# Kernel tuning notes

Measured on AMD Instinct MI355X. Metric: run time of the kernel, lower is better.

The kernel has to match this reference:

```python
import jax, jax.numpy as jnp
import numpy as np

B, N_PER, DEG = 1024, 256, 16
N = B * N_PER            # 262144 total nodes
E = B * N_PER * DEG      # 4194304 edges
F_IN, H, K, C = 7, 64, 50, 2


def setup_inputs() -> dict:
    key = jax.random.key(0)
    ks = jax.random.split(key, 16)
    rng = np.random.default_rng(0)
    # within-graph random edges: nodes of graph g occupy [g*N_PER, (g+1)*N_PER)
    offs = np.repeat(np.arange(B, dtype=np.int64) * N_PER, N_PER * DEG)
    src = offs + rng.integers(0, N_PER, size=E)
    dst = offs + rng.integers(0, N_PER, size=E)
    edge_index = jnp.asarray(np.stack([src, dst]), dtype=jnp.int64)
    batch = jnp.repeat(jnp.arange(B, dtype=jnp.int64), N_PER)
    sc = lambda fan: 1.0 / np.sqrt(fan)
    return {
        'x': jax.random.normal(ks[0], (N, F_IN), jnp.float32),
        'W1a': jax.random.normal(ks[1], (F_IN, H), jnp.float32) * sc(F_IN),
        'b1a': jnp.zeros((H,), jnp.float32),
        'W1b': jax.random.normal(ks[2], (H, H), jnp.float32) * sc(H),
        'b1b': jnp.zeros((H,), jnp.float32),
        'Wp': jax.random.normal(ks[3], (H, K), jnp.float32) * sc(H),
        'bp': jnp.zeros((K,), jnp.float32),
        'W2a': jax.random.normal(ks[4], (H, H), jnp.float32) * sc(H),
        'b2a': jnp.zeros((H,), jnp.float32),
        'W2b': jax.random.normal(ks[5], (H, H), jnp.float32) * sc(H),
        'b2b': jnp.zeros((H,), jnp.float32),
        'Wl': jax.random.normal(ks[6], (H, C), jnp.float32) * sc(H),
        'bl': jnp.zeros((C,), jnp.float32),
        'edge_index': edge_index,
        'batch': batch,
    }


def reference(x, W1a, b1a, W1b, b1b, Wp, bp, W2a, b2a, W2b, b2b, Wl, bl,
              edge_index, batch):
    src, dst = edge_index[0], edge_index[1]
    # --- sparse GINConv (eps=0): MLP(x + sum_{j in N(i)} x_j) ---
    agg = jnp.zeros_like(x).at[dst].add(x[src])          # scatter-add over edges
    h = jax.nn.relu((x + agg) @ W1a + b1a) @ W1b + b1b   # [N, H]
    # --- densify per graph (equal-size contiguous graphs) ---
    xd = h.reshape(B, N_PER, H)                          # [B, n, H]
    g = src // N_PER
    si = src % N_PER
    di = dst % N_PER
    A = jnp.zeros((B, N_PER, N_PER), x.dtype).at[g, si, di].add(1.0)
    # --- BNPool-style soft cluster pooling ---
    S = jax.nn.softmax(xd @ Wp + bp, axis=-1)            # [B, n, K]
    xp = jnp.einsum('bnk,bnd->bkd', S, xd)               # [B, K, H]
    AS = jnp.einsum('bnm,bmk->bnk', A, S)
    Ap = jnp.einsum('bnk,bnl->bkl', S, AS)               # [B, K, K]
    SSt = jnp.einsum('bnk,bmk->bnm', S, S)
    link_loss = jnp.sqrt(jnp.sum((A - SSt) ** 2)) / A.size
    ent_loss = -jnp.mean(jnp.sum(S * jnp.log(S + 1e-15), axis=-1))
    aux_loss = link_loss + ent_loss
    # --- DenseGINConv (eps=0): MLP(x + A @ x) ---
    h2 = xp + jnp.einsum('bkl,bld->bkd', Ap, xp)
    h2 = jax.nn.relu(h2 @ W2a + b2a) @ W2b + b2b         # [B, K, H]
    # --- mean pool over clusters + classifier ---
    logits = h2.mean(axis=1) @ Wl + bl                   # [B, C]
    return jax.nn.log_softmax(logits, axis=-1), aux_loss
```

## Files before the change

### kernel.cpp

```cpp
#include <hip/hip_runtime.h>
#include <math.h>

#define NG   1024
#define NP   256
#define EPG  4096
#define ETOT 4194304
#define FIN  7
#define HD   64
#define KC   50
#define FST  72
#define TST  264
#define AST2 132
#define TSC  0.00390625f
#define TSCI 256.0f

#define SW_ST(k, n)  ((k) * 256 + ((n) ^ (((k) & 7) << 3)))
#define SW_AW(r, w)  ((r) * 128 + ((w) ^ (((r) & 7) << 2)))
#define SW_AH(r, h)  ((r) * 256 + ((h) ^ (((r) & 7) << 3)))


typedef __attribute__((ext_vector_type(8))) _Float16 v8h;
typedef __attribute__((ext_vector_type(4))) float v4f;

__global__ void finalize_k(const float* __restrict__ ws, float* __restrict__ out) {
    if (threadIdx.x == 0) {
        float num = ws[0] - 2.f * ws[2] + ws[3];
        float link = sqrtf(fmaxf(num, 0.f)) / 67108864.0f;
        float ent  = -ws[1] / 262144.0f;
        out[2048] = link + ent;
    }
}

__device__ __forceinline__ float blockReduceN(float v, float* red, int nw) {
    __syncthreads();
    #pragma unroll
    for (int o = 32; o > 0; o >>= 1) v += __shfl_down(v, o);
    if ((threadIdx.x & 63) == 0) red[threadIdx.x >> 6] = v;
    __syncthreads();
    float r = 0.f;
    if (threadIdx.x == 0) {
        for (int i = 0; i < nw; ++i) r += red[i];
    }
    return r;
}

__device__ __forceinline__ void blockReduce3(float& a, float& b, float& c,
                                             float* red) {
    __syncthreads();
    #pragma unroll
    for (int o = 32; o > 0; o >>= 1) {
        a += __shfl_down(a, o);
        b += __shfl_down(b, o);
        c += __shfl_down(c, o);
    }
    const int wid = threadIdx.x >> 6;
    if ((threadIdx.x & 63) == 0) {
        red[wid * 3] = a; red[wid * 3 + 1] = b; red[wid * 3 + 2] = c;
    }
    __syncthreads();
    if (threadIdx.x == 0) {
        float ra = 0.f, rb = 0.f, rc = 0.f;
        for (int i = 0; i < 16; ++i) {
            ra += red[i * 3]; rb += red[i * 3 + 1]; rc += red[i * 3 + 2];
        }
        a = ra; b = rb; c = rc;
    }
}

__launch_bounds__(1024, 1)
__global__ void mega(const int* __restrict__ esrc, const int* __restrict__ edst,
                     const float* __restrict__ x,
                     const float* __restrict__ W1a, const float* __restrict__ b1a,
                     const float* __restrict__ W1b, const float* __restrict__ b1b,
                     const float* __restrict__ Wp,  const float* __restrict__ bp,
                     const float* __restrict__ W2a, const float* __restrict__ b2a,
                     const float* __restrict__ W2b, const float* __restrict__ b2b,
                     const float* __restrict__ Wl,  const float* __restrict__ bl,
                     float* __restrict__ out, float* __restrict__ ws)
{
    __shared__ __align__(16) _Float16 ST[64 * 256];
    __shared__ __align__(16) _Float16 xagg[NP * 8];
    __shared__ __align__(16) _Float16 W1bT[64 * FST];
    __shared__ __align__(16) _Float16 WWT[64 * FST];
    __shared__ __align__(16) _Float16 W2aT[64 * FST];
    __shared__ __align__(16) _Float16 W2bT[64 * FST];
    __shared__ float bPl[64];
    __shared__ __align__(16) union {
        struct {
            unsigned char ssi[EPG];
            float xt8[NP * 8];
            unsigned int hist[256], cur[256], roff[NP + 1];
        } k1;
        struct {
            unsigned char pad[16384];
            _Float16 WpT_s[64 * FST];
            _Float16 W1bN[64 * FST];
        } w;
        struct {
            _Float16 t1b[NP * FST];
            _Float16 t1T[HD * TST];
        } k2;
        struct {
            unsigned int cnt[128 * 128];
            _Float16 T1T[64 * AST2];
        } a;
        struct {
            _Float16 Apf_tf[64 * FST];
            _Float16 xpT[64 * FST];
            _Float16 h2f[64 * FST];
        } b;
    } u;
    __shared__ float cs[64];
    __shared__ float red[48];

    const int g = blockIdx.x, tid = threadIdx.x;
    const int lane = tid & 63, wid = tid >> 6;
    const int l15 = lane & 15, quad = lane >> 4, fko = quad * 8;
    const int mt = (wid >> 2) << 4, nt = (wid & 3) << 4;

    for (int i = tid; i < 64 * 128; i += 1024) ((unsigned int*)ST)[i] = 0u;
    for (int i = tid; i < 64 * FST / 2; i += 1024) ((unsigned int*)u.w.WpT_s)[i] = 0u;
    if (tid < 256) u.k1.hist[tid] = 0u;
    __syncthreads();

    unsigned int cellr[4];
    #pragma unroll
    for (int j = 0; j < 4; ++j) {
        int e = tid + j * 1024;
        int s = esrc[g * EPG + e] & (NP - 1);
        int d = edst[g * EPG + e] & (NP - 1);
        cellr[j] = (unsigned)((s << 8) | d);
        atomicAdd(&u.k1.hist[d], 1u);
    }
    for (int i = tid; i < NP * 8; i += 1024) {
        int n = i >> 3, f = i & 7;
        u.k1.xt8[i] = (f < FIN) ? x[g * NP * FIN + n * FIN + f] : 0.f;
    }
    #pragma unroll
    for (int j = 0; j < 4; ++j) {
        int i = tid + j * 1024;
        int a0 = i >> 6, b0 = i & 63;
        W1bT[b0 * FST + a0] = (_Float16)W1b[i];
        u.w.W1bN[a0 * FST + b0] = (_Float16)W1b[i];
        W2aT[b0 * FST + a0] = (_Float16)W2a[i];
        W2bT[b0 * FST + a0] = (_Float16)W2b[i];
    }
    for (int i = tid; i < HD * KC; i += 1024) {
        int h2 = i / KC, k = i - h2 * KC;
        u.w.WpT_s[k * FST + h2] = (_Float16)Wp[i];
    }
    __syncthreads();

    if (wid == 0) {
        unsigned carry = 0;
        for (int c = 0; c < 4; ++c) {
            unsigned v = u.k1.hist[c * 64 + lane];
            unsigned s = v;
            #pragma unroll
            for (int o = 1; o < 64; o <<= 1) {
                unsigned t = __shfl_up(s, o);
                if (lane >= o) s += t;
            }
            unsigned excl = s - v + carry;
            u.k1.roff[c * 64 + lane] = excl;
            u.k1.cur[c * 64 + lane] = excl;
            carry += __shfl(s, 63);
        }
        if (lane == 0) u.k1.roff[NP] = EPG;
    }
    {
        v4f acc = {0.f, 0.f, 0.f, 0.f};
        #pragma unroll
        for (int ks = 0; ks < 2; ++ks) {
            v8h af = *(const v8h*)&u.w.WpT_s[(mt + l15) * FST + ks * 32 + fko];
            v8h bf = *(const v8h*)&u.w.W1bN[(nt + l15) * FST + ks * 32 + fko];
            acc = __builtin_amdgcn_mfma_f32_16x16x32_f16(af, bf, acc, 0, 0, 0);
        }
        #pragma unroll
        for (int r = 0; r < 4; ++r)
            WWT[(mt + quad * 4 + r) * FST + nt + l15] = (_Float16)acc[r];
    }
    {
        int k = tid >> 4, q = tid & 15;
        float v = 0.f;
        #pragma unroll
        for (int d0 = 0; d0 < 4; ++d0) {
            int d = q * 4 + d0;
            v += b1b[d] * (float)u.w.WpT_s[k * FST + d];
        }
        #pragma unroll
        for (int o = 8; o > 0; o >>= 1) v += __shfl_xor(v, o);
        if (q == 0) bPl[k] = v + ((k < KC) ? bp[k] : 0.f);
    }
    __syncthreads();

    #pragma unroll
    for (int j = 0; j < 4; ++j) {
        unsigned c = cellr[j];
        unsigned p2 = atomicAdd(&u.k1.cur[c & 255u], 1u);
        u.k1.ssi[p2] = (unsigned char)(c >> 8);
    }
    __syncthreads();

    {
        const int gi = tid >> 3, f = tid & 7;
        for (int n = gi; n < NP; n += 128) {
            int beg = u.k1.roff[n], end = u.k1.roff[n + 1];
            float a = u.k1.xt8[n * 8 + f];
            for (int e = beg; e < end; ++e)
                a += u.k1.xt8[u.k1.ssi[e] * 8 + f];
            xagg[n * 8 + f] = (_Float16)a;
        }
    }
    __syncthreads();

    {
        float w1r[FIN];
        #pragma unroll
        for (int f = 0; f < FIN; ++f) w1r[f] = W1a[f * HD + lane];
        float b1r = b1a[lane];
        for (int it = 0; it < 16; ++it) {
            int n = it * 16 + wid;
            float a = b1r;
            #pragma unroll
            for (int f = 0; f < FIN; ++f)
                a += (float)xagg[n * 8 + f] * w1r[f];
            _Float16 tv = (_Float16)fmaxf(a, 0.f);
            u.k2.t1b[n * FST + lane] = tv;
            u.k2.t1T[lane * TST + n] = tv;
        }
    }
    __syncthreads();

    float entL = 0.f;
    {
        const int r16 = wid << 4;
        v4f pa[4];
        #pragma unroll
        for (int c = 0; c < 4; ++c) {
            v4f acc = {0.f, 0.f, 0.f, 0.f};
            #pragma unroll
            for (int ks = 0; ks < 2; ++ks) {
                v8h af = *(const v8h*)&u.k2.t1b[(r16 + l15) * FST + ks * 32 + fko];
                v8h bf = *(const v8h*)&WWT[(c * 16 + l15) * FST + ks * 32 + fko];
                acc = __builtin_amdgcn_mfma_f32_16x16x32_f16(af, bf, acc, 0, 0, 0);
            }
            pa[c] = acc;
        }
        float bv[4]; bool valid[4];
        #pragma unroll
        for (int c = 0; c < 4; ++c) {
            int col = c * 16 + l15;
            bv[c] = bPl[col];
            valid[c] = col < KC;
        }
        #pragma unroll
        for (int r = 0; r < 4; ++r) {
            float pv[4];
            #pragma unroll
            for (int c = 0; c < 4; ++c)
                pv[c] = valid[c] ? (pa[c][r] + bv[c]) : -INFINITY;
            float m = fmaxf(fmaxf(pv[0], pv[1]), fmaxf(pv[2], pv[3]));
            #pragma unroll
            for (int o = 8; o > 0; o >>= 1) m = fmaxf(m, __shfl_xor(m, o));
            float e[4], Z = 0.f;
            #pragma unroll
            for (int c = 0; c < 4; ++c) {
                e[c] = valid[c] ? __expf(pv[c] - m) : 0.f;
                Z += e[c];
            }
            #pragma unroll
            for (int o = 8; o > 0; o >>= 1) Z += __shfl_xor(Z, o);
            float zi = 1.f / Z, lZ = __logf(Z);
            int row = r16 + quad * 4 + r;
            #pragma unroll
            for (int c = 0; c < 4; ++c) {
                if (valid[c]) {
                    float s = e[c] * zi;
                    ST[SW_ST(c * 16 + l15, row)] = (_Float16)s;
                    entL += s * (pv[c] - m);
                }
            }
            if (l15 == 0) entL -= lZ;
        }
    }
    __syncthreads();

    v4f spa = {0.f, 0.f, 0.f, 0.f};
    {
        const int ar = mt + l15, br = nt + l15;
        #pragma unroll
        for (int ks = 0; ks < 8; ++ks) {
            int ko = ks * 32 + fko;
            v8h af = *(const v8h*)&ST[SW_ST(ar, ko)];
            v8h bf = *(const v8h*)&u.k2.t1T[br * TST + ko];
            spa = __builtin_amdgcn_mfma_f32_16x16x32_f16(af, bf, spa, 0, 0, 0);
        }
    }
    {
        _Float16* SPb = u.k2.t1b;
        int c = nt + l15;
        #pragma unroll
        for (int r = 0; r < 4; ++r)
            SPb[(mt + quad * 4 + r) * FST + c] = (_Float16)spa[r];
    }
    {
        int k = tid >> 4, q = tid & 15;
        float v = 0.f;
        #pragma unroll
        for (int i = 0; i < 16; ++i) v += (float)ST[SW_ST(k, q * 16 + i)];
        #pragma unroll
        for (int o = 8; o > 0; o >>= 1) v += __shfl_xor(v, o);
        if (q == 0) cs[k] = v;
    }
    {
        float rE = blockReduceN(entL, red, 16);
        if (tid == 0) atomicAdd(&ws[1], rE);
    }

    v4f axp;
    {
        const int d = nt + l15;
        float bv = b1b[d];
        #pragma unroll
        for (int r = 0; r < 4; ++r) axp[r] = cs[mt + quad * 4 + r] * bv;
        #pragma unroll
        for (int ks = 0; ks < 2; ++ks) {
            v8h af = *(const v8h*)&u.k2.t1b[(mt + l15) * FST + ks * 32 + fko];
            v8h bf = *(const v8h*)&W1bT[(nt + l15) * FST + ks * 32 + fko];
            axp = __builtin_amdgcn_mfma_f32_16x16x32_f16(af, bf, axp, 0, 0, 0);
        }
    }
    __syncthreads();

    float sumA2 = 0.f;
    v4f ap = {0.f, 0.f, 0.f, 0.f};
    v4f ag = {0.f, 0.f, 0.f, 0.f};

    for (int i = tid; i < 128 * 128; i += 1024) u.a.cnt[i] = 0u;
    __syncthreads();

    for (int ch = 0; ch < 2; ++ch) {
        int rlo = ch << 7;
        #pragma unroll
        for (int j = 0; j < 4; ++j) {
            unsigned c = cellr[j];
            int sr = (int)(c >> 8) - rlo;
            if ((unsigned)sr < 128u) {
                int d = c & 255u;
                atomicAdd(&u.a.cnt[SW_AW(sr, d >> 1)],
                          (d & 1) ? 0x10000u : 1u);
            }
        }
        __syncthreads();

        for (int i = tid; i < 128 * 128; i += 1024) {
            unsigned v = u.a.cnt[i];
            float m0 = (float)(v & 0xffffu), m1 = (float)(v >> 16);
            sumA2 += m0 * m0 + m1 * m1;
            union { unsigned uu; _Float16 h[2]; } cv;
            cv.h[0] = (_Float16)m0; cv.h[1] = (_Float16)m1;
            u.a.cnt[i] = cv.uu;
        }
        __syncthreads();

        const _Float16* Af = (const _Float16*)u.a.cnt;

        #pragma unroll
        for (int tt = 0; tt < 2; ++tt) {
            int t = wid + tt * 16;
            int mt3 = (t >> 2) << 4, nt3 = (t & 3) << 4;
            v4f acc = {0.f, 0.f, 0.f, 0.f};
            #pragma unroll
            for (int ks = 0; ks < 8; ++ks) {
                v8h af = *(const v8h*)&Af[SW_AH(mt3 + l15, ks * 32 + fko)];
                v8h bf = *(const v8h*)&ST[SW_ST(nt3 + l15, ks * 32 + fko)];
                acc = __builtin_amdgcn_mfma_f32_16x16x32_f16(af, bf, acc, 0, 0, 0);
            }
            int c = nt3 + l15;
            #pragma unroll
            for (int r = 0; r < 4; ++r)
                u.a.T1T[c * AST2 + mt3 + quad * 4 + r] = (_Float16)acc[r];
        }
        __syncthreads();

        {
            const int ar = mt + l15, br = nt + l15;
            #pragma unroll
            for (int ks = 0; ks < 4; ++ks) {
                int ko = (ch << 7) + ks * 32 + fko;
                v8h af = *(const v8h*)&ST[SW_ST(ar, ko)];
                v8h bt = *(const v8h*)&u.a.T1T[br * AST2 + ks * 32 + fko];
                v8h bs = *(const v8h*)&ST[SW_ST(br, ko)];
                ap = __builtin_amdgcn_mfma_f32_16x16x32_f16(af, bt, ap, 0, 0, 0);
                ag = __builtin_amdgcn_mfma_f32_16x16x32_f16(af, bs, ag, 0, 0, 0);
            }
        }
        if (ch < 1) {
            for (int i = tid; i < 128 * 128; i += 1024) u.a.cnt[i] = 0u;
        }
        __syncthreads();
    }

    float tr = 0.f, g2 = 0.f;
    {
        int c = nt + l15;
        #pragma unroll
        for (int r = 0; r < 4; ++r) {
            int k = mt + quad * 4 + r;
            u.b.Apf_tf[k * FST + c] = (_Float16)ap[r];
            u.b.xpT[c * FST + k] = (_Float16)axp[r];
            if (k < KC && c < KC) {
                if (k == c) tr += ap[r];
                g2 += ag[r] * ag[r];
            }
        }
    }

    blockReduce3(sumA2, tr, g2, red);
    if (tid == 0) {
        atomicAdd(&ws[0], sumA2);
        atomicAdd(&ws[2], tr);
        atomicAdd(&ws[3], g2);
    }
    __syncthreads();

    {
        v4f hacc = axp;
        #pragma unroll
        for (int ks = 0; ks < 2; ++ks) {
            v8h af = *(const v8h*)&u.b.Apf_tf[(mt + l15) * FST + ks * 32 + fko];
            v8h bf = *(const v8h*)&u.b.xpT[(nt + l15) * FST + ks * 32 + fko];
            hacc = __builtin_amdgcn_mfma_f32_16x16x32_f16(af, bf, hacc, 0, 0, 0);
        }
        int d = nt + l15;
        #pragma unroll
        for (int r = 0; r < 4; ++r)
            u.b.h2f[(mt + quad * 4 + r) * FST + d] = (_Float16)(hacc[r] * TSC);
    }
    __syncthreads();

    {
        float bv = b2a[nt + l15] * TSC;
        v4f tacc = {bv, bv, bv, bv};
        #pragma unroll
        for (int ks = 0; ks < 2; ++ks) {
            v8h af = *(const v8h*)&u.b.h2f[(mt + l15) * FST + ks * 32 + fko];
            v8h bf = *(const v8h*)&W2aT[(nt + l15) * FST + ks * 32 + fko];
            tacc = __builtin_amdgcn_mfma_f32_16x16x32_f16(af, bf, tacc, 0, 0, 0);
        }
        int d2 = nt + l15;
        #pragma unroll
        for (int r = 0; r < 4; ++r)
            u.b.Apf_tf[(mt + quad * 4 + r) * FST + d2] = (_Float16)fmaxf(tacc[r], 0.f);
    }
    __syncthreads();

    float l0 = 0.f, l1 = 0.f;
    {
        v4f oacc = {0.f, 0.f, 0.f, 0.f};
        #pragma unroll
        for (int ks = 0; ks < 2; ++ks) {
            v8h af = *(const v8h*)&u.b.Apf_tf[(mt + l15) * FST + ks * 32 + fko];
            v8h bf = *(const v8h*)&W2bT[(nt + l15) * FST + ks * 32 + fko];
            oacc = __builtin_amdgcn_mfma_f32_16x16x32_f16(af, bf, oacc, 0, 0, 0);
        }
        int j = nt + l15;
        float bv = b2b[j];
        float wl0 = Wl[j * 2], wl1 = Wl[j * 2 + 1];
        #pragma unroll
        for (int r = 0; r < 4; ++r) {
            int k = mt + quad * 4 + r;
            if (k < KC) {
                float h3v = oacc[r] * TSCI + bv;
                l0 += h3v * wl0; l1 += h3v * wl1;
            }
        }
    }

    float dummy = 0.f;
    blockReduce3(l0, l1, dummy, red);
    if (tid == 0) {
        float g0 = bl[0] + l0 * (1.f / KC);
        float g1 = bl[1] + l1 * (1.f / KC);
        float mm = fmaxf(g0, g1);
        float lse = mm + __logf(__expf(g0 - mm) + __expf(g1 - mm));
        out[2 * g]     = g0 - lse;
        out[2 * g + 1] = g1 - lse;
    }
}

extern "C" void kernel_launch(void* const* d_in, const int* in_sizes, int n_in,
                              void* d_out, int out_size, void* d_ws, size_t ws_size,
                              hipStream_t stream) {
    const float* x    = (const float*)d_in[0];
    const float* W1a  = (const float*)d_in[1];
    const float* b1a  = (const float*)d_in[2];
    const float* W1b  = (const float*)d_in[3];
    const float* b1b  = (const float*)d_in[4];
    const float* Wp   = (const float*)d_in[5];
    const float* bp   = (const float*)d_in[6];
    const float* W2a  = (const float*)d_in[7];
    const float* b2a  = (const float*)d_in[8];
    const float* W2b  = (const float*)d_in[9];
    const float* b2b  = (const float*)d_in[10];
    const float* Wl   = (const float*)d_in[11];
    const float* bl   = (const float*)d_in[12];
    const int*   eidx = (const int*)d_in[13];
    float* out = (float*)d_out;
    float* ws  = (float*)d_ws;

    hipMemsetAsync(ws, 0, 4 * sizeof(float), stream);
    mega<<<NG, 1024, 0, stream>>>(eidx, eidx + ETOT, x,
                                  W1a, b1a, W1b, b1b, Wp, bp,
                                  W2a, b2a, W2b, b2b, Wl, bl, out, ws);
    finalize_k<<<1, 64, 0, stream>>>(ws, out);
}
```

Baseline: 239.7 us.

## Merge block reductions, trim zero-fills, vectorize edge loads, split gather across lanes

Consolidates four separate block reductions (entropy, link terms, logits) into a single shuffle+LDS reduction at the end, removing several barriers. Zero-initializes only the padding rows of ST and WpT_s instead of the full buffers, loads edge indices as int4, and splits each node's neighbor gather across two lane halves combined with a shuffle. It also reorders the adjacency-count histogram and the Apf/xp staging so they share barriers with neighbouring work. This adds complexity, and correctness now depends on the non-padded rows always being fully overwritten.

Result: no change. 243.8 us (+1.7%).

```diff
diff --git a/kernel.cpp b/kernel.cpp
--- a/kernel.cpp
+++ b/kernel.cpp
@@ -28,42 +28,6 @@
         float link = sqrtf(fmaxf(num, 0.f)) / 67108864.0f;
         float ent  = -ws[1] / 262144.0f;
         out[2048] = link + ent;
-    }
-}
-
-__device__ __forceinline__ float blockReduceN(float v, float* red, int nw) {
-    __syncthreads();
-    #pragma unroll
-    for (int o = 32; o > 0; o >>= 1) v += __shfl_down(v, o);
-    if ((threadIdx.x & 63) == 0) red[threadIdx.x >> 6] = v;
-    __syncthreads();
-    float r = 0.f;
-    if (threadIdx.x == 0) {
-        for (int i = 0; i < nw; ++i) r += red[i];
-    }
-    return r;
-}
-
-__device__ __forceinline__ void blockReduce3(float& a, float& b, float& c,
-                                             float* red) {
-    __syncthreads();
-    #pragma unroll
-    for (int o = 32; o > 0; o >>= 1) {
-        a += __shfl_down(a, o);
-        b += __shfl_down(b, o);
-        c += __shfl_down(c, o);
-    }
-    const int wid = threadIdx.x >> 6;
-    if ((threadIdx.x & 63) == 0) {
-        red[wid * 3] = a; red[wid * 3 + 1] = b; red[wid * 3 + 2] = c;
-    }
-    __syncthreads();
-    if (threadIdx.x == 0) {
-        float ra = 0.f, rb = 0.f, rc = 0.f;
-        for (int i = 0; i < 16; ++i) {
-            ra += red[i * 3]; rb += red[i * 3 + 1]; rc += red[i * 3 + 2];
-        }
-        a = ra; b = rb; c = rc;
     }
 }
 
@@ -111,26 +75,27 @@
         } b;
     } u;
     __shared__ float cs[64];
-    __shared__ float red[48];
+    __shared__ float red[96];
 
     const int g = blockIdx.x, tid = threadIdx.x;
     const int lane = tid & 63, wid = tid >> 6;
     const int l15 = lane & 15, quad = lane >> 4, fko = quad * 8;
     const int mt = (wid >> 2) << 4, nt = (wid & 3) << 4;
 
-    for (int i = tid; i < 64 * 128; i += 1024) ((unsigned int*)ST)[i] = 0u;
-    for (int i = tid; i < 64 * FST / 2; i += 1024) ((unsigned int*)u.w.WpT_s)[i] = 0u;
     if (tid < 256) u.k1.hist[tid] = 0u;
     __syncthreads();
 
     unsigned int cellr[4];
-    #pragma unroll
-    for (int j = 0; j < 4; ++j) {
-        int e = tid + j * 1024;
-        int s = esrc[g * EPG + e] & (NP - 1);
-        int d = edst[g * EPG + e] & (NP - 1);
-        cellr[j] = (unsigned)((s << 8) | d);
-        atomicAdd(&u.k1.hist[d], 1u);
+    {
+        int4 sv = ((const int4*)(esrc + g * EPG))[tid];
+        int4 dv = ((const int4*)(edst + g * EPG))[tid];
+        int ss[4] = {sv.x & (NP-1), sv.y & (NP-1), sv.z & (NP-1), sv.w & (NP-1)};
+        int dd[4] = {dv.x & (NP-1), dv.y & (NP-1), dv.z & (NP-1), dv.w & (NP-1)};
+        #pragma unroll
+        for (int j = 0; j < 4; ++j) {
+            cellr[j] = (unsigned)((ss[j] << 8) | dd[j]);
+            atomicAdd(&u.k1.hist[dd[j]], 1u);
+        }
     }
     for (int i = tid; i < NP * 8; i += 1024) {
         int n = i >> 3, f = i & 7;
@@ -149,6 +114,12 @@
         int h2 = i / KC, k = i - h2 * KC;
         u.w.WpT_s[k * FST + h2] = (_Float16)Wp[i];
     }
+    for (int i = tid; i < 14 * 64; i += 1024) {
+        int k = 50 + (i >> 6), h2 = i & 63;
+        u.w.WpT_s[k * FST + h2] = (_Float16)0.f;
+    }
+    for (int i = tid; i < 14 * 128; i += 1024)
+        ((unsigned int*)ST)[(50 + (i >> 7)) * 128 + (i & 127)] = 0u;
     __syncthreads();
 
     if (wid == 0) {
@@ -203,13 +174,14 @@
     __syncthreads();
 
     {
-        const int gi = tid >> 3, f = tid & 7;
-        for (int n = gi; n < NP; n += 128) {
+        const int gi = tid >> 4, f = tid & 7, hv = (tid >> 3) & 1;
+        for (int n = gi; n < NP; n += 64) {
             int beg = u.k1.roff[n], end = u.k1.roff[n + 1];
-            float a = u.k1.xt8[n * 8 + f];
-            for (int e = beg; e < end; ++e)
+            float a = hv ? 0.f : u.k1.xt8[n * 8 + f];
+            for (int e = beg + hv; e < end; e += 2)
                 a += u.k1.xt8[u.k1.ssi[e] * 8 + f];
-            xagg[n * 8 + f] = (_Float16)a;
+            a += __shfl_xor(a, 8);
+            if (hv == 0) xagg[n * 8 + f] = (_Float16)a;
         }
     }
     __syncthreads();
@@ -286,8 +258,8 @@
     }
     __syncthreads();
 
-    v4f spa = {0.f, 0.f, 0.f, 0.f};
-    {
+    {
+        v4f spa = {0.f, 0.f, 0.f, 0.f};
         const int ar = mt + l15, br = nt + l15;
         #pragma unroll
         for (int ks = 0; ks < 8; ++ks) {
@@ -296,13 +268,10 @@
             v8h bf = *(const v8h*)&u.k2.t1T[br * TST + ko];
             spa = __builtin_amdgcn_mfma_f32_16x16x32_f16(af, bf, spa, 0, 0, 0);
         }
-    }
-    {
-        _Float16* SPb = u.k2.t1b;
         int c = nt + l15;
         #pragma unroll
         for (int r = 0; r < 4; ++r)
-            SPb[(mt + quad * 4 + r) * FST + c] = (_Float16)spa[r];
+            WWT[(mt + quad * 4 + r) * FST + c] = (_Float16)spa[r];
     }
     {
         int k = tid >> 4, q = tid & 15;
@@ -313,10 +282,10 @@
         for (int o = 8; o > 0; o >>= 1) v += __shfl_xor(v, o);
         if (q == 0) cs[k] = v;
     }
-    {
-        float rE = blockReduceN(entL, red, 16);
-        if (tid == 0) atomicAdd(&ws[1], rE);
-    }
+    __syncthreads();
+
+    for (int i = tid; i < 128 * 128; i += 1024) u.a.cnt[i] = 0u;
+    __syncthreads();
 
     v4f axp;
     {
@@ -326,34 +295,28 @@
         for (int r = 0; r < 4; ++r) axp[r] = cs[mt + quad * 4 + r] * bv;
         #pragma unroll
         for (int ks = 0; ks < 2; ++ks) {
-            v8h af = *(const v8h*)&u.k2.t1b[(mt + l15) * FST + ks * 32 + fko];
+            v8h af = *(const v8h*)&WWT[(mt + l15) * FST + ks * 32 + fko];
             v8h bf = *(const v8h*)&W1bT[(nt + l15) * FST + ks * 32 + fko];
             axp = __builtin_amdgcn_mfma_f32_16x16x32_f16(af, bf, axp, 0, 0, 0);
         }
     }
-    __syncthreads();
-
     float sumA2 = 0.f;
     v4f ap = {0.f, 0.f, 0.f, 0.f};
     v4f ag = {0.f, 0.f, 0.f, 0.f};
-
-    for (int i = tid; i < 128 * 128; i += 1024) u.a.cnt[i] = 0u;
+    float tr = 0.f, g2 = 0.f, l0 = 0.f, l1 = 0.f;
+
+    #pragma unroll
+    for (int j = 0; j < 4; ++j) {
+        unsigned c = cellr[j];
+        int sr = (int)(c >> 8);
+        if (sr < 128) {
+            int d = c & 255u;
+            atomicAdd(&u.a.cnt[SW_AW(sr, d >> 1)], (d & 1) ? 0x10000u : 1u);
+        }
+    }
     __syncthreads();
 
     for (int ch = 0; ch < 2; ++ch) {
-        int rlo = ch << 7;
-        #pragma unroll
-        for (int j = 0; j < 4; ++j) {
-            unsigned c = cellr[j];
-            int sr = (int)(c >> 8) - rlo;
-            if ((unsigned)sr < 128u) {
-                int d = c & 255u;
-                atomicAdd(&u.a.cnt[SW_AW(sr, d >> 1)],
-                          (d & 1) ? 0x10000u : 1u);
-            }
-        }
-        __syncthreads();
-
         for (int i = tid; i < 128 * 128; i += 1024) {
             unsigned v = u.a.cnt[i];
             float m0 = (float)(v & 0xffffu), m1 = (float)(v >> 16);
@@ -396,34 +359,35 @@
                 ag = __builtin_amdgcn_mfma_f32_16x16x32_f16(af, bs, ag, 0, 0, 0);
             }
         }
-        if (ch < 1) {
+        if (ch == 0) {
             for (int i = tid; i < 128 * 128; i += 1024) u.a.cnt[i] = 0u;
-        }
-        __syncthreads();
-    }
-
-    float tr = 0.f, g2 = 0.f;
-    {
-        int c = nt + l15;
-        #pragma unroll
-        for (int r = 0; r < 4; ++r) {
-            int k = mt + quad * 4 + r;
-            u.b.Apf_tf[k * FST + c] = (_Float16)ap[r];
-            u.b.xpT[c * FST + k] = (_Float16)axp[r];
-            if (k < KC && c < KC) {
-                if (k == c) tr += ap[r];
-                g2 += ag[r] * ag[r];
-            }
-        }
-    }
-
-    blockReduce3(sumA2, tr, g2, red);
-    if (tid == 0) {
-        atomicAdd(&ws[0], sumA2);
-        atomicAdd(&ws[2], tr);
-        atomicAdd(&ws[3], g2);
-    }
-    __syncthreads();
+            __syncthreads();
+            #pragma unroll
+            for (int j = 0; j < 4; ++j) {
+                unsigned c = cellr[j];
+                int sr = (int)(c >> 8) - 128;
+                if (sr >= 0) {
+                    int d = c & 255u;
+                    atomicAdd(&u.a.cnt[SW_AW(sr, d >> 1)],
+                              (d & 1) ? 0x10000u : 1u);
+                }
+            }
+            __syncthreads();
+        } else {
+            int c = nt + l15;
+            #pragma unroll
+            for (int r = 0; r < 4; ++r) {
+                int k = mt + quad * 4 + r;
+                u.b.Apf_tf[k * FST + c] = (_Float16)ap[r];
+                u.b.xpT[c * FST + k] = (_Float16)axp[r];
+                if (k < KC && c < KC) {
+                    if (k == c) tr += ap[r];
+                    g2 += ag[r] * ag[r];
+                }
+            }
+            __syncthreads();
+        }
+    }
 
     {
         v4f hacc = axp;
@@ -456,7 +420,6 @@
     }
     __syncthreads();
 
-    float l0 = 0.f, l1 = 0.f;
     {
         v4f oacc = {0.f, 0.f, 0.f, 0.f};
         #pragma unroll
@@ -478,11 +441,34 @@
         }
     }
 
-    float dummy = 0.f;
-    blockReduce3(l0, l1, dummy, red);
+    #pragma unroll
+    for (int o = 32; o > 0; o >>= 1) {
+        sumA2 += __shfl_down(sumA2, o);
+        entL  += __shfl_down(entL,  o);
+        tr    += __shfl_down(tr,    o);
+        g2    += __shfl_down(g2,    o);
+        l0    += __shfl_down(l0,    o);
+        l1    += __shfl_down(l1,    o);
+    }
+    if (lane == 0) {
+        red[wid * 6 + 0] = sumA2; red[wid * 6 + 1] = entL;
+        red[wid * 6 + 2] = tr;    red[wid * 6 + 3] = g2;
+        red[wid * 6 + 4] = l0;    red[wid * 6 + 5] = l1;
+    }
+    __syncthreads();
     if (tid == 0) {
-        float g0 = bl[0] + l0 * (1.f / KC);
-        float g1 = bl[1] + l1 * (1.f / KC);
+        float s0 = 0.f, s1 = 0.f, s2 = 0.f, s3 = 0.f, s4 = 0.f, s5 = 0.f;
+        for (int i = 0; i < 16; ++i) {
+            s0 += red[i * 6];     s1 += red[i * 6 + 1];
+            s2 += red[i * 6 + 2]; s3 += red[i * 6 + 3];
+            s4 += red[i * 6 + 4]; s5 += red[i * 6 + 5];
+        }
+        atomicAdd(&ws[0], s0);
+        atomicAdd(&ws[1], s1);
+        atomicAdd(&ws[2], s2);
+        atomicAdd(&ws[3], s3);
+        float g0 = bl[0] + s4 * (1.f / KC);
+        float g1 = bl[1] + s5 * (1.f / KC);
         float mm = fmaxf(g0, g1);
         float lse = mm + __logf(__expf(g0 - mm) + __expf(g1 - mm));
         out[2 * g]     = g0 - lse;
```
